# Optimization experiments

Measured on AMD Instinct MI355X. Metric: run time of the kernel, lower is better.

Reference implementation:

```python
import jax, jax.numpy as jnp
import numpy as np

NEG_SLOPE = 0.2


def gat_conv(x, src, dst, W, a_src, a_dst, b, n_nodes):
    # h: [N, F_out] projected node features
    h = x @ W
    # per-node attention halves (PyG: alpha = a_src.h_i + a_dst.h_j)
    s_src = h @ a_src  # [N]
    s_dst = h @ a_dst  # [N]
    # per-edge raw score, leaky relu
    e = s_src[src] + s_dst[dst]  # [E]
    e = jnp.where(e >= 0, e, NEG_SLOPE * e)
    # softmax grouped by destination node (stable via segment max)
    m = jax.ops.segment_max(e, dst, num_segments=n_nodes)  # [N]
    ex = jnp.exp(e - m[dst])
    z = jax.ops.segment_sum(ex, dst, num_segments=n_nodes)  # [N]
    alpha = ex / z[dst]  # [E]  (z>0: self-loops guarantee >=1 incoming edge)
    # weighted scatter-add of source messages
    out = jax.ops.segment_sum(h[src] * alpha[:, None], dst, num_segments=n_nodes)
    return out + b


def setup_inputs() -> dict:
    key = jax.random.key(0)
    ks = jax.random.split(key, 10)
    N, E, F_in, H, C = 100000, 1600000, 128, 128, 2
    x = jax.random.normal(ks[0], (N, F_in), dtype=jnp.float32)
    edge_index = jax.random.randint(ks[1], (2, E), 0, N, dtype=jnp.int64)
    sc = 1.0 / np.sqrt(F_in)
    W1 = jax.random.normal(ks[2], (F_in, H), dtype=jnp.float32) * sc
    a_src1 = jax.random.normal(ks[3], (H,), dtype=jnp.float32) * sc
    a_dst1 = jax.random.normal(ks[4], (H,), dtype=jnp.float32) * sc
    b1 = jnp.zeros((H,), dtype=jnp.float32)
    sc2 = 1.0 / np.sqrt(H)
    W2 = jax.random.normal(ks[5], (H, C), dtype=jnp.float32) * sc2
    a_src2 = jax.random.normal(ks[6], (C,), dtype=jnp.float32) * sc2
    a_dst2 = jax.random.normal(ks[7], (C,), dtype=jnp.float32) * sc2
    b2 = jnp.zeros((C,), dtype=jnp.float32)
    return {"x": x, "edge_index": edge_index, "W1": W1, "a_src1": a_src1,
            "a_dst1": a_dst1, "b1": b1, "W2": W2, "a_src2": a_src2,
            "a_dst2": a_dst2, "b2": b2}


def reference(x, edge_index, W1, a_src1, a_dst1, b1, W2, a_src2, a_dst2, b2):
    N = x.shape[0]
    # add self-loops (PyG GATConv default add_self_loops=True)
    loop = jnp.arange(N, dtype=edge_index.dtype)
    src = jnp.concatenate([edge_index[0], loop])
    dst = jnp.concatenate([edge_index[1], loop])
    h = gat_conv(x, src, dst, W1, a_src1, a_dst1, b1, N)
    h = jax.nn.relu(h)
    out = gat_conv(h, src, dst, W2, a_src2, a_dst2, b2, N)
    return out
```

## Files before the change

kernel.cpp:

```cpp
#include <hip/hip_runtime.h>
#include <hip/hip_bf16.h>

#define PAD 64
#define BN 128
#define BSH 7
#define CAP 3072
#define RPT4 8
#define MAXB 800

typedef short bf16x8 __attribute__((ext_vector_type(8)));
typedef float f32x4  __attribute__((ext_vector_type(4)));
typedef int   i32x4  __attribute__((ext_vector_type(4)));

__device__ __forceinline__ unsigned short f2bf(float f) {
    unsigned u = __float_as_uint(f);
    u += 0x7fffu + ((u >> 16) & 1u);
    return (unsigned short)(u >> 16);
}
__device__ __forceinline__ float bl(unsigned v) { return __uint_as_float(v << 16); }
__device__ __forceinline__ float bh(unsigned v) { return __uint_as_float(v & 0xffff0000u); }


__global__ void setup_kernel(const float* __restrict__ W1, unsigned short* __restrict__ Bp,
                             int* __restrict__ gbase, int nbucket) {
    int i = blockIdx.x * blockDim.x + threadIdx.x;
    if (blockIdx.x < 64) {
        int j    = i & 7;
        int lane = (i >> 3) & 63;
        int ks   = (i >> 9) & 3;
        int n    = i >> 11;
        int k = ks * 32 + (lane >> 4) * 8 + j;
        int c = n * 16 + (lane & 15);
        Bp[i] = f2bf(W1[k * 128 + c]);
    } else {
        int b = i - 64 * 256;
        if (b < nbucket) gbase[b] = b * CAP;
    }
}


__global__ __launch_bounds__(256) void partA_kernel(const int* __restrict__ ei,
                                                    int* __restrict__ gbase,
                                                    long long* __restrict__ segbuf,
                                                    int E, int nbucket) {
    __shared__ int cnt[MAXB];
    __shared__ int base[MAXB];
    const i32x4* s4p = (const i32x4*)ei;
    const i32x4* d4p = (const i32x4*)(ei + E);
    int E4 = E >> 2;
    int i0 = blockIdx.x * (256 * RPT4);
    for (int i = threadIdx.x; i < nbucket; i += 256) cnt[i] = 0;
    __syncthreads();
    i32x4 sv[RPT4], dv[RPT4];
    bool ok[RPT4];
#pragma unroll
    for (int w = 0; w < RPT4; ++w) {
        int idx = i0 + w * 256 + (int)threadIdx.x;
        ok[w] = idx < E4;
        sv[w] = (i32x4){0, 0, 0, 0};
        dv[w] = (i32x4){0, 0, 0, 0};
        if (ok[w]) {
            sv[w] = __builtin_nontemporal_load(s4p + idx);
            dv[w] = __builtin_nontemporal_load(d4p + idx);
        }
    }
#pragma unroll
    for (int w = 0; w < RPT4; ++w) {
        if (ok[w]) {
            atomicAdd(&cnt[dv[w][0] >> BSH], 1);
            atomicAdd(&cnt[dv[w][1] >> BSH], 1);
            atomicAdd(&cnt[dv[w][2] >> BSH], 1);
            atomicAdd(&cnt[dv[w][3] >> BSH], 1);
        }
    }
    __syncthreads();
    for (int i = threadIdx.x; i < nbucket; i += 256) {
        int c = cnt[i];
        base[i] = c ? atomicAdd(&gbase[i], c) : 0;
        cnt[i] = 0;
    }
    __syncthreads();
#pragma unroll
    for (int w = 0; w < RPT4; ++w) {
        if (ok[w]) {
#pragma unroll
            for (int j = 0; j < 4; ++j) {
                int dst = dv[w][j], src = sv[w][j];
                int b = dst >> BSH;
                int r = atomicAdd(&cnt[b], 1);
                int pos = base[b] + r;
                if (pos < (b + 1) * CAP)
                    segbuf[pos] = ((long long)dst << 32) | (unsigned)src;
            }
        }
    }
}


__global__ __launch_bounds__(256) void fusedBG_kernel(
        const int* __restrict__ gbase, const long long* __restrict__ segbuf,
        int* __restrict__ esrc, int* __restrict__ deg, int Nn, int nbucket,
        const float* __restrict__ A, const unsigned short* __restrict__ Bp,
        const float* __restrict__ a_src, const float* __restrict__ a_dst,
        unsigned short* __restrict__ Cb, float* __restrict__ ssrc,
        float* __restrict__ sdst) {
    __shared__ char smem[BN * 4 + BN * PAD * 4];
    int t = threadIdx.x;

    if ((int)blockIdx.x < nbucket) {
        int* lcnt = (int*)smem;
        int* lrow = (int*)(smem + BN * 4);
        int b = blockIdx.x;
        int node0 = b << BSH;
        int cnt = gbase[b] - b * CAP; if (cnt > CAP) cnt = CAP;
        for (int i = t; i < BN; i += 256) {
            lcnt[i] = 1;
            lrow[i * PAD] = node0 + i;
        }
        __syncthreads();
        const long long* buf = segbuf + (size_t)b * CAP;
        for (int i = t; i < cnt; i += 256) {
            long long v = buf[i];
            int src = (int)(v & 0xffffffffLL);
            int ld  = ((int)(v >> 32)) & (BN - 1);
            int r = atomicAdd(&lcnt[ld], 1);
            if (r < PAD) lrow[ld * PAD + r] = src;
        }
        __syncthreads();
        int4* gout = (int4*)(esrc + (size_t)node0 * PAD);
        const int4* lin = (const int4*)lrow;
        int maxv = (BN * PAD) / 4;
        int lim = ((Nn - node0) * PAD) / 4;
        if (lim < maxv) maxv = lim;
        for (int i = t; i < maxv; i += 256)
            gout[i] = lin[i];
        if (t < BN) {
            int node = node0 + t;
            if (node < Nn) {
                int d = lcnt[t];
                deg[node] = (d < PAD) ? d : PAD;
            }
        }
        return;
    }

    unsigned short* Ct = (unsigned short*)smem;
    int wid = t >> 6, lane = t & 63;
    int lq = lane & 15;
    int kg = lane >> 4;
    int m0 = ((int)blockIdx.x - nbucket) * 64;
    int row = m0 + wid * 16 + lq;
    int M = Nn;
    bool rok = row < M;

    bf16x8 afr[4];
    const float* arow = A + (size_t)row * 128;
#pragma unroll
    for (int ks = 0; ks < 4; ++ks) {
        float4 f0 = make_float4(0.f, 0.f, 0.f, 0.f), f1 = f0;
        if (rok) {
            f0 = *(const float4*)(arow + ks * 32 + kg * 8);
            f1 = *(const float4*)(arow + ks * 32 + kg * 8 + 4);
        }
        union { unsigned short us[8]; bf16x8 v; } pk;
        pk.us[0] = f2bf(f0.x); pk.us[1] = f2bf(f0.y); pk.us[2] = f2bf(f0.z); pk.us[3] = f2bf(f0.w);
        pk.us[4] = f2bf(f1.x); pk.us[5] = f2bf(f1.y); pk.us[6] = f2bf(f1.z); pk.us[7] = f2bf(f1.w);
        afr[ks] = pk.v;
    }

    f32x4 acc[8];
#pragma unroll
    for (int n = 0; n < 8; ++n) acc[n] = (f32x4){0.f, 0.f, 0.f, 0.f};

    const bf16x8* bfr = (const bf16x8*)Bp;
#pragma unroll
    for (int ks = 0; ks < 4; ++ks) {
#pragma unroll
        for (int n = 0; n < 8; ++n) {
            bf16x8 b = bfr[(n * 4 + ks) * 64 + lane];
            acc[n] = __builtin_amdgcn_mfma_f32_16x16x32_bf16(afr[ks], b, acc[n], 0, 0, 0);
        }
    }

    float psr[4] = {0.f, 0.f, 0.f, 0.f}, pdr[4] = {0.f, 0.f, 0.f, 0.f};
#pragma unroll
    for (int n = 0; n < 8; ++n) {
        float as_ = a_src[n * 16 + lq];
        float ad_ = a_dst[n * 16 + lq];
#pragma unroll
        for (int r = 0; r < 4; ++r) { psr[r] += acc[n][r] * as_; pdr[r] += acc[n][r] * ad_; }
    }
#pragma unroll
    for (int off = 1; off < 16; off <<= 1) {
#pragma unroll
        for (int r = 0; r < 4; ++r) {
            psr[r] += __shfl_xor(psr[r], off);
            pdr[r] += __shfl_xor(pdr[r], off);
        }
    }
    if (lq == 0) {
#pragma unroll
        for (int r = 0; r < 4; ++r) {
            int gr = m0 + wid * 16 + kg * 4 + r;
            if (gr < M) { ssrc[gr] = psr[r]; sdst[gr] = pdr[r]; }
        }
    }

#pragma unroll
    for (int n = 0; n < 8; ++n) {
#pragma unroll
        for (int r = 0; r < 4; ++r)
            Ct[(wid * 16 + kg * 4 + r) * 128 + n * 16 + lq] = f2bf(acc[n][r]);
    }
    __syncthreads();
    {
        int r = t >> 2, sg = t & 3;
        int gr = m0 + r;
        if (gr < M) {
            const uint4* srcp = (const uint4*)(Ct + r * 128 + sg * 32);
            uint4* dstp = (uint4*)(Cb + (size_t)gr * 128 + sg * 32);
            dstp[0] = srcp[0]; dstp[1] = srcp[1]; dstp[2] = srcp[2]; dstp[3] = srcp[3];
        }
    }
}


__global__ void agg1_kernel(const unsigned short* __restrict__ hb,
                            const float* __restrict__ ssrc,
                            const float* __restrict__ sdst, const int* __restrict__ deg,
                            const int* __restrict__ esrc, const float* __restrict__ b1,
                            const float* __restrict__ W2, const float* __restrict__ as2,
                            const float* __restrict__ ad2,
                            float* __restrict__ h2, float* __restrict__ ss2,
                            float* __restrict__ sd2, int N) {
    __shared__ int   sm_s[4][64];
    __shared__ float sm_e[4][64];
    int wid  = threadIdx.x >> 6;
    int node = (blockIdx.x * blockDim.x + threadIdx.x) >> 6;
    int lane = threadIdx.x & 63;
    if (node >= N) return;
    int nk = deg[node]; if (nk > PAD) nk = PAD;
    const int* rowp = esrc + (size_t)node * PAD;
    float sd = sdst[node];
    int s = 0; float ex = 0.f;
    if (lane < nk) {
        s = rowp[lane];
        float e = ssrc[s] + sd;
        e = (e >= 0.f) ? e : 0.2f * e;
        ex = __expf(e);
    }
    sm_s[wid][lane] = s;
    sm_e[wid][lane] = ex;
    float z = ex;
#pragma unroll
    for (int off = 32; off; off >>= 1) z += __shfl_xor(z, off);

    int g = lane >> 4, q = lane & 15;
    const unsigned short* hq = hb + q * 8;
    float a[8];
#pragma unroll
    for (int j = 0; j < 8; ++j) a[j] = 0.f;

#define ACC8(u, e)                                         \
    { a[0] += (e) * bl((u).x); a[1] += (e) * bh((u).x);    \
      a[2] += (e) * bl((u).y); a[3] += (e) * bh((u).y);    \
      a[4] += (e) * bl((u).z); a[5] += (e) * bh((u).z);    \
      a[6] += (e) * bl((u).w); a[7] += (e) * bh((u).w); }

    for (int kb = 0; kb < nk; kb += 32) {
        uint4 u0, u1, u2, u3, u4, u5, u6, u7;
        u0 = *(const uint4*)(hq + (size_t)sm_s[wid][kb + 0  + g] * 128);
        if (kb +  4 < nk) u1 = *(const uint4*)(hq + (size_t)sm_s[wid][kb + 4  + g] * 128);
        if (kb +  8 < nk) u2 = *(const uint4*)(hq + (size_t)sm_s[wid][kb + 8  + g] * 128);
        if (kb + 12 < nk) u3 = *(const uint4*)(hq + (size_t)sm_s[wid][kb + 12 + g] * 128);
        if (kb + 16 < nk) u4 = *(const uint4*)(hq + (size_t)sm_s[wid][kb + 16 + g] * 128);
        if (kb + 20 < nk) u5 = *(const uint4*)(hq + (size_t)sm_s[wid][kb + 20 + g] * 128);
        if (kb + 24 < nk) u6 = *(const uint4*)(hq + (size_t)sm_s[wid][kb + 24 + g] * 128);
        if (kb + 28 < nk) u7 = *(const uint4*)(hq + (size_t)sm_s[wid][kb + 28 + g] * 128);
        {                 float e = sm_e[wid][kb + 0  + g]; ACC8(u0, e); }
        if (kb +  4 < nk) { float e = sm_e[wid][kb + 4  + g]; ACC8(u1, e); }
        if (kb +  8 < nk) { float e = sm_e[wid][kb + 8  + g]; ACC8(u2, e); }
        if (kb + 12 < nk) { float e = sm_e[wid][kb + 12 + g]; ACC8(u3, e); }
        if (kb + 16 < nk) { float e = sm_e[wid][kb + 16 + g]; ACC8(u4, e); }
        if (kb + 20 < nk) { float e = sm_e[wid][kb + 20 + g]; ACC8(u5, e); }
        if (kb + 24 < nk) { float e = sm_e[wid][kb + 24 + g]; ACC8(u6, e); }
        if (kb + 28 < nk) { float e = sm_e[wid][kb + 28 + g]; ACC8(u7, e); }
    }
#undef ACC8
#pragma unroll
    for (int j = 0; j < 8; ++j) {
        a[j] += __shfl_xor(a[j], 16);
        a[j] += __shfl_xor(a[j], 32);
    }
    float inv = 1.f / z;
    float4 b1a = ((const float4*)b1)[2 * q];
    float4 b1b = ((const float4*)b1)[2 * q + 1];
    float o[8];
    o[0] = a[0] * inv + b1a.x; o[1] = a[1] * inv + b1a.y;
    o[2] = a[2] * inv + b1a.z; o[3] = a[3] * inv + b1a.w;
    o[4] = a[4] * inv + b1b.x; o[5] = a[5] * inv + b1b.y;
    o[6] = a[6] * inv + b1b.z; o[7] = a[7] * inv + b1b.w;
#pragma unroll
    for (int j = 0; j < 8; ++j) o[j] = (o[j] > 0.f) ? o[j] : 0.f;
    float p0 = 0.f, p1 = 0.f;
#pragma unroll
    for (int j = 0; j < 8; ++j) {
        float2 wv = ((const float2*)W2)[8 * q + j];
        p0 += o[j] * wv.x;
        p1 += o[j] * wv.y;
    }
#pragma unroll
    for (int off = 1; off < 16; off <<= 1) {
        p0 += __shfl_xor(p0, off);
        p1 += __shfl_xor(p1, off);
    }
    if (lane == 0) {
        ((float2*)h2)[node] = make_float2(p0, p1);
        ss2[node] = p0 * as2[0] + p1 * as2[1];
        sd2[node] = p0 * ad2[0] + p1 * ad2[1];
    }
}


__global__ void agg2_kernel(const float* __restrict__ h2, const float* __restrict__ ss2,
                            const float* __restrict__ sd2, const int* __restrict__ deg,
                            const int* __restrict__ esrc, const float* __restrict__ b2,
                            float* __restrict__ out, int N) {
    int node = (blockIdx.x * blockDim.x + threadIdx.x) >> 6;
    int lane = threadIdx.x & 63;
    if (node >= N) return;
    int nk = deg[node]; if (nk > PAD) nk = PAD;
    const int* row = esrc + (size_t)node * PAD;
    float sd = sd2[node];
    float z = 0.f, a0 = 0.f, a1 = 0.f;
    if (lane < nk) {
        int s = row[lane];
        float e = ss2[s] + sd;
        e = (e >= 0.f) ? e : 0.2f * e;
        float ex = __expf(e);
        z = ex;
        float2 hv = ((const float2*)h2)[s];
        a0 = ex * hv.x;
        a1 = ex * hv.y;
    }
#pragma unroll
    for (int off = 32; off; off >>= 1) {
        z  += __shfl_xor(z, off);
        a0 += __shfl_xor(a0, off);
        a1 += __shfl_xor(a1, off);
    }
    if (lane == 0) {
        float inv = 1.f / z;
        out[2 * (size_t)node + 0] = a0 * inv + b2[0];
        out[2 * (size_t)node + 1] = a1 * inv + b2[1];
    }
}


extern "C" void kernel_launch(void* const* d_in, const int* in_sizes, int n_in,
                              void* d_out, int out_size, void* d_ws, size_t ws_size,
                              hipStream_t stream) {
    const float* x      = (const float*)d_in[0];
    const int*   ei     = (const int*)d_in[1];
    const float* W1     = (const float*)d_in[2];
    const float* a_src1 = (const float*)d_in[3];
    const float* a_dst1 = (const float*)d_in[4];
    const float* b1     = (const float*)d_in[5];
    const float* W2     = (const float*)d_in[6];
    const float* a_src2 = (const float*)d_in[7];
    const float* a_dst2 = (const float*)d_in[8];
    const float* b2     = (const float*)d_in[9];
    float* out = (float*)d_out;

    int N  = in_sizes[0] / 128;
    int E  = in_sizes[1] / 2;
    int nbucket = (N >> BSH) + ((N & (BN - 1)) ? 1 : 0);

    char* w = (char*)d_ws;
    auto alloc = [&](size_t bytes) -> void* {
        void* p = (void*)w;
        w += (bytes + 255) & ~(size_t)255;
        return p;
    };
    unsigned short* h1 = (unsigned short*)alloc((size_t)N * 128 * 2);
    unsigned short* Bp = (unsigned short*)alloc(16384 * 2);
    float* ss1    = (float*)alloc((size_t)N * 4);
    float* sd1    = (float*)alloc((size_t)N * 4);
    float* h2     = (float*)alloc((size_t)N * 2 * 4);
    float* ss2    = (float*)alloc((size_t)N * 4);
    float* sd2    = (float*)alloc((size_t)N * 4);
    int*   deg    = (int*)alloc((size_t)N * 4);
    int*   gbase  = (int*)alloc((size_t)MAXB * 4);
    long long* segbuf = (long long*)alloc((size_t)nbucket * CAP * 8);
    int*   esrc   = (int*)alloc((size_t)N * PAD * 4);

    const int tb = 256;
    int E4 = E >> 2;
    int nblkA = (E4 + 256 * RPT4 - 1) / (256 * RPT4);
    int nblkG = (N + 63) / 64;

    setup_kernel<<<64 + 4, tb, 0, stream>>>(W1, Bp, gbase, nbucket);
    partA_kernel<<<nblkA, tb, 0, stream>>>(ei, gbase, segbuf, E, nbucket);
    fusedBG_kernel<<<nbucket + nblkG, tb, 0, stream>>>(gbase, segbuf, esrc, deg, N, nbucket,
                                                       x, Bp, a_src1, a_dst1, h1, ss1, sd1);
    agg1_kernel<<<(N + 3) / 4, 256, 0, stream>>>(h1, ss1, sd1, deg, esrc, b1,
                                                 W2, a_src2, a_dst2, h2, ss2, sd2, N);
    agg2_kernel<<<(N + 3) / 4, 256, 0, stream>>>(h2, ss2, sd2, deg, esrc, b2, out, N);
}
```

Before: 149.8 us.

## Merge setup into partition kernel, memset bucket bases, half-wave agg2 per node

```diff
diff --git a/kernel.cpp b/kernel.cpp
--- a/kernel.cpp
+++ b/kernel.cpp
@@ -21,10 +21,14 @@
 __device__ __forceinline__ float bh(unsigned v) { return __uint_as_float(v & 0xffff0000u); }
 
 
-__global__ void setup_kernel(const float* __restrict__ W1, unsigned short* __restrict__ Bp,
-                             int* __restrict__ gbase, int nbucket) {
-    int i = blockIdx.x * blockDim.x + threadIdx.x;
+__global__ __launch_bounds__(256) void partA_kernel(const int* __restrict__ ei,
+                                                    int* __restrict__ gbase,
+                                                    long long* __restrict__ segbuf,
+                                                    const float* __restrict__ W1,
+                                                    unsigned short* __restrict__ Bp,
+                                                    int E, int nbucket) {
     if (blockIdx.x < 64) {
+        int i = blockIdx.x * 256 + threadIdx.x;
         int j    = i & 7;
         int lane = (i >> 3) & 63;
         int ks   = (i >> 9) & 3;
@@ -32,23 +36,14 @@
         int k = ks * 32 + (lane >> 4) * 8 + j;
         int c = n * 16 + (lane & 15);
         Bp[i] = f2bf(W1[k * 128 + c]);
-    } else {
-        int b = i - 64 * 256;
-        if (b < nbucket) gbase[b] = b * CAP;
-    }
-}
-
-
-__global__ __launch_bounds__(256) void partA_kernel(const int* __restrict__ ei,
-                                                    int* __restrict__ gbase,
-                                                    long long* __restrict__ segbuf,
-                                                    int E, int nbucket) {
+        return;
+    }
     __shared__ int cnt[MAXB];
     __shared__ int base[MAXB];
     const i32x4* s4p = (const i32x4*)ei;
     const i32x4* d4p = (const i32x4*)(ei + E);
     int E4 = E >> 2;
-    int i0 = blockIdx.x * (256 * RPT4);
+    int i0 = ((int)blockIdx.x - 64) * (256 * RPT4);
     for (int i = threadIdx.x; i < nbucket; i += 256) cnt[i] = 0;
     __syncthreads();
     i32x4 sv[RPT4], dv[RPT4];
@@ -76,7 +71,7 @@
     __syncthreads();
     for (int i = threadIdx.x; i < nbucket; i += 256) {
         int c = cnt[i];
-        base[i] = c ? atomicAdd(&gbase[i], c) : 0;
+        base[i] = c ? (i * CAP + atomicAdd(&gbase[i], c)) : 0;
         cnt[i] = 0;
     }
     __syncthreads();
@@ -112,7 +107,7 @@
         int* lrow = (int*)(smem + BN * 4);
         int b = blockIdx.x;
         int node0 = b << BSH;
-        int cnt = gbase[b] - b * CAP; if (cnt > CAP) cnt = CAP;
+        int cnt = gbase[b]; if (cnt > CAP) cnt = CAP;
         for (int i = t; i < BN; i += 256) {
             lcnt[i] = 1;
             lrow[i * PAD] = node0 + i;
@@ -154,17 +149,17 @@
     bool rok = row < M;
 
     bf16x8 afr[4];
-    const float* arow = A + (size_t)row * 128;
+    const f32x4* arow4 = (const f32x4*)(A + (size_t)row * 128);
 #pragma unroll
     for (int ks = 0; ks < 4; ++ks) {
-        float4 f0 = make_float4(0.f, 0.f, 0.f, 0.f), f1 = f0;
+        f32x4 f0 = (f32x4){0.f, 0.f, 0.f, 0.f}, f1 = f0;
         if (rok) {
-            f0 = *(const float4*)(arow + ks * 32 + kg * 8);
-            f1 = *(const float4*)(arow + ks * 32 + kg * 8 + 4);
+            f0 = __builtin_nontemporal_load(arow4 + ks * 8 + kg * 2);
+            f1 = __builtin_nontemporal_load(arow4 + ks * 8 + kg * 2 + 1);
         }
         union { unsigned short us[8]; bf16x8 v; } pk;
-        pk.us[0] = f2bf(f0.x); pk.us[1] = f2bf(f0.y); pk.us[2] = f2bf(f0.z); pk.us[3] = f2bf(f0.w);
-        pk.us[4] = f2bf(f1.x); pk.us[5] = f2bf(f1.y); pk.us[6] = f2bf(f1.z); pk.us[7] = f2bf(f1.w);
+        pk.us[0] = f2bf(f0[0]); pk.us[1] = f2bf(f0[1]); pk.us[2] = f2bf(f0[2]); pk.us[3] = f2bf(f0[3]);
+        pk.us[4] = f2bf(f1[0]); pk.us[5] = f2bf(f1[1]); pk.us[6] = f2bf(f1[2]); pk.us[7] = f2bf(f1[3]);
         afr[ks] = pk.v;
     }
 
@@ -326,30 +321,31 @@
                             const float* __restrict__ sd2, const int* __restrict__ deg,
                             const int* __restrict__ esrc, const float* __restrict__ b2,
                             float* __restrict__ out, int N) {
-    int node = (blockIdx.x * blockDim.x + threadIdx.x) >> 6;
-    int lane = threadIdx.x & 63;
+    int tid  = blockIdx.x * blockDim.x + threadIdx.x;
+    int node = (tid >> 6) * 2 + ((tid & 63) >> 5);
+    int hl   = tid & 31;
     if (node >= N) return;
     int nk = deg[node]; if (nk > PAD) nk = PAD;
     const int* row = esrc + (size_t)node * PAD;
     float sd = sd2[node];
     float z = 0.f, a0 = 0.f, a1 = 0.f;
-    if (lane < nk) {
-        int s = row[lane];
+    for (int k = hl; k < nk; k += 32) {
+        int s = __builtin_nontemporal_load(row + k);
         float e = ss2[s] + sd;
         e = (e >= 0.f) ? e : 0.2f * e;
         float ex = __expf(e);
-        z = ex;
+        z += ex;
         float2 hv = ((const float2*)h2)[s];
-        a0 = ex * hv.x;
-        a1 = ex * hv.y;
-    }
-#pragma unroll
-    for (int off = 32; off; off >>= 1) {
+        a0 += ex * hv.x;
+        a1 += ex * hv.y;
+    }
+#pragma unroll
+    for (int off = 16; off; off >>= 1) {
         z  += __shfl_xor(z, off);
         a0 += __shfl_xor(a0, off);
         a1 += __shfl_xor(a1, off);
     }
-    if (lane == 0) {
+    if (hl == 0) {
         float inv = 1.f / z;
         out[2 * (size_t)node + 0] = a0 * inv + b2[0];
         out[2 * (size_t)node + 1] = a1 * inv + b2[1];
@@ -399,11 +395,11 @@
     int nblkA = (E4 + 256 * RPT4 - 1) / (256 * RPT4);
     int nblkG = (N + 63) / 64;
 
-    setup_kernel<<<64 + 4, tb, 0, stream>>>(W1, Bp, gbase, nbucket);
-    partA_kernel<<<nblkA, tb, 0, stream>>>(ei, gbase, segbuf, E, nbucket);
+    (void)hipMemsetAsync(gbase, 0, (size_t)nbucket * 4, stream);
+    partA_kernel<<<64 + nblkA, tb, 0, stream>>>(ei, gbase, segbuf, W1, Bp, E, nbucket);
     fusedBG_kernel<<<nbucket + nblkG, tb, 0, stream>>>(gbase, segbuf, esrc, deg, N, nbucket,
                                                        x, Bp, a_src1, a_dst1, h1, ss1, sd1);
     agg1_kernel<<<(N + 3) / 4, 256, 0, stream>>>(h1, ss1, sd1, deg, esrc, b1,
                                                  W2, a_src2, a_dst2, h2, ss2, sd2, N);
-    agg2_kernel<<<(N + 3) / 4, 256, 0, stream>>>(h2, ss2, sd2, deg, esrc, b2, out, N);
-}
+    agg2_kernel<<<(N + 7) / 8, 256, 0, stream>>>(h2, ss2, sd2, deg, esrc, b2, out, N);
+}
```

Result: no change. 147.9 us (-1.3%).
